# Kernel tuning notes

Measured on AMD Instinct MI355X. Metric: run time of the kernel, lower is better.

## Reference

```python
import jax, jax.numpy as jnp
import numpy as np

BN_EPS = 1e-5


def setup_inputs() -> dict:
    key = jax.random.key(0)
    k1, k2, k3, k4 = jax.random.split(key, 4)
    N, C, T, V, K = 64, 128, 300, 25, 3
    x = jax.random.normal(k1, (N, C, T, V), dtype=jnp.float32)
    A = jax.random.uniform(k2, (K, V, V), dtype=jnp.float32)
    # 1x1 conv weight (out_channels*K, in_channels) and bias
    W = jax.random.normal(k3, (C * K, C), dtype=jnp.float32) * 0.05
    b = jax.random.normal(k4, (C * K,), dtype=jnp.float32) * 0.05
    gamma = jnp.ones((C,), dtype=jnp.float32)
    beta = jnp.zeros((C,), dtype=jnp.float32)
    return {"x": x, "A": A, "W": W, "b": b, "gamma": gamma, "beta": beta}


def reference(x, A, W, b, gamma, beta):
    N, C, T, V = x.shape
    K = A.shape[0]
    # 1x1 conv: expand channels C -> K*C
    y = jnp.einsum('nctv,oc->notv', x, W) + b[None, :, None, None]
    y = y.reshape(N, K, C, T, V)
    # graph aggregation over K adjacency matrices
    y = jnp.einsum('nkctv,kvw->nctw', y, A)
    # residual + relu
    y = jax.nn.relu(y + x)
    # BatchNorm2d (training mode): stats over (N, T, V) per channel, biased var
    mean = jnp.mean(y, axis=(0, 2, 3), keepdims=True)
    var = jnp.mean(jnp.square(y - mean), axis=(0, 2, 3), keepdims=True)
    out = gamma[None, :, None, None] * (y - mean) * jax.lax.rsqrt(var + BN_EPS) + beta[None, :, None, None]
    return out, A
```

## Files before the change

kernel.cpp:

```cpp
#include <hip/hip_runtime.h>
#include <cstdint>
#include <cstddef>

#define C_    128
#define T_    300
#define V_    25
#define TT    2
#define KA    3
#define KDIM  384
#define B2P   136
#define ALP   40
#define XTP   40
#define NSLOT 64
#define NTOT  64

#define ALBF_O 0
#define XT_O   3840
#define B2_O   14080
#define SH_TOT 22784

typedef __attribute__((ext_vector_type(8))) short short8;
typedef __attribute__((ext_vector_type(4))) short short4v;
typedef __attribute__((ext_vector_type(4))) float float4v;
typedef __attribute__((ext_vector_type(2))) float float2v;

__device__ __forceinline__ short f2bf(float f) {
  union { float f; uint32_t u; } v; v.f = f;
  uint32_t r = (v.u + 0x7FFFu + ((v.u >> 16) & 1u)) >> 16;
  return (short)(uint16_t)r;
}
__device__ __forceinline__ float bf2f(short s) {
  union { uint32_t u; float f; } v; v.u = ((uint32_t)(uint16_t)s) << 16;
  return v.f;
}

__global__ __launch_bounds__(256) void k0_prep(const float* __restrict__ W,
    const float* __restrict__ A, const float* __restrict__ b,
    short* __restrict__ W2, float* __restrict__ bias2, float* __restrict__ stats)
{
  int e = blockIdx.x * 256 + threadIdx.x;
  if (e < C_*KDIM) {
    int c = e / KDIM, kd = e % KDIM;
    int k = kd >> 7, c2 = kd & 127;
    W2[e] = f2bf(W[(k*C_ + c)*C_ + c2]);
  } else if (e < C_*KDIM + C_*32) {
    int i = e - C_*KDIM;
    int c = i >> 5, w = i & 31;
    float val = 0.f;
    if (w < V_) {
      for (int k = 0; k < KA; ++k) {
        float cs = 0.f;
        for (int v = 0; v < V_; ++v) cs += A[(k*V_ + v)*V_ + w];
        val += b[k*C_ + c] * cs;
      }
    }
    bias2[i] = val;
  } else if (e < C_*KDIM + C_*32 + 2*NSLOT*C_) {
    stats[e - (C_*KDIM + C_*32)] = 0.f;
  }
}

__global__ __launch_bounds__(256, 3) void k1_main(const float* __restrict__ x,
    const float* __restrict__ A, const short* __restrict__ W2,
    const float* __restrict__ bias2, float* __restrict__ ssum,
    float* __restrict__ ssq, float* __restrict__ out)
{
  __shared__ __align__(16) short SH[SH_TOT];
  short* Albf_ = SH + ALBF_O;
  short* xt_   = SH + XT_O;
  short* B2_   = SH + B2_O;

  const int tid  = threadIdx.x;
  const int lane = tid & 63;
  const int wid  = tid >> 6;
  const int l15  = lane & 15;
  const int quad = lane >> 4;
  const int nb = blockIdx.x;
  const int n  = nb / (T_/TT);
  const int tb = nb % (T_/TT);
  const int t0 = tb * TT;

  for (int i = tid; i < KA*32*ALP; i += 256) {
    int k = i / (32*ALP);
    int rem = i % (32*ALP);
    int w = rem / ALP;
    int v = rem % ALP;
    float a = (w < V_ && v < V_) ? A[(k*V_ + v)*V_ + w] : 0.f;
    Albf_[i] = f2bf(a);
  }
  for (int i = tid; i < TT*C_*15; i += 256) {
    int t = i / (C_*15);
    int r = i % (C_*15);
    int c = r / 15;
    int v = V_ + (r % 15);
    xt_[t*5120 + c*XTP + v] = 0;
  }
  {
    const float* xb = x + (((size_t)n*C_)*T_ + t0)*V_;
    for (int p = tid; p < 3200; p += 256) {
      int c = (p*5243) >> 17;
      int r = p - c*25;
      float2v xv = *(const float2v*)(xb + (size_t)c*(T_*V_) + 2*r);
      int j0 = 2*r;
      { int j = j0;   int t = (j >= V_); int v = j - t*V_; xt_[t*5120 + c*XTP + v] = f2bf(xv[0]); }
      { int j = j0+1; int t = (j >= V_); int v = j - t*V_; xt_[t*5120 + c*XTP + v] = f2bf(xv[1]); }
    }
  }
  __syncthreads();

  const int mh = wid >> 1;
  const int tW = wid & 1;
  const int wm = wid >> 1;
  const int wn = wid & 1;

  float4v acc[4][2];
  #pragma unroll
  for (int mi = 0; mi < 4; ++mi)
    #pragma unroll
    for (int ni = 0; ni < 2; ++ni)
      acc[mi][ni] = (float4v){0.f, 0.f, 0.f, 0.f};

  short8 w2r[4][4];
  const short* w2base = W2 + (size_t)(wm*64 + l15)*KDIM + quad*8;

  for (int k = 0; k < KA; ++k) {
    #pragma unroll
    for (int ks = 0; ks < 4; ++ks)
      #pragma unroll
      for (int mi = 0; mi < 4; ++mi)
        w2r[ks][mi] = *(const short8*)(w2base + (size_t)mi*16*KDIM + k*C_ + ks*32);

    {
      short8 bf0 = *(const short8*)&Albf_[k*1280 + l15*ALP + quad*8];
      short8 bf1 = *(const short8*)&Albf_[k*1280 + (16 + l15)*ALP + quad*8];
      #pragma unroll
      for (int mi4 = 0; mi4 < 4; ++mi4) {
        int m8 = mh*4 + mi4;
        short8 af = *(const short8*)&xt_[tW*5120 + (m8*16 + l15)*XTP + quad*8];
        int c2 = m8*16 + quad*4;
        #pragma unroll
        for (int ni = 0; ni < 2; ++ni) {
          float4v s1 = {0.f, 0.f, 0.f, 0.f};
          s1 = __builtin_amdgcn_mfma_f32_16x16x32_bf16(af, ni ? bf1 : bf0, s1, 0, 0, 0);
          short4v sv;
          sv[0] = f2bf(s1[0]); sv[1] = f2bf(s1[1]);
          sv[2] = f2bf(s1[2]); sv[3] = f2bf(s1[3]);
          int pos = tW*32 + ni*16 + l15;
          *(short4v*)&B2_[pos*B2P + c2] = sv;
        }
      }
    }
    __syncthreads();

    #pragma unroll
    for (int ks = 0; ks < 4; ++ks) {
      short8 b0 = *(const short8*)&B2_[(wn*32 + l15)*B2P + ks*32 + quad*8];
      short8 b1 = *(const short8*)&B2_[(wn*32 + 16 + l15)*B2P + ks*32 + quad*8];
      #pragma unroll
      for (int mi = 0; mi < 4; ++mi) {
        acc[mi][0] = __builtin_amdgcn_mfma_f32_16x16x32_bf16(w2r[ks][mi], b0, acc[mi][0], 0, 0, 0);
        acc[mi][1] = __builtin_amdgcn_mfma_f32_16x16x32_bf16(w2r[ks][mi], b1, acc[mi][1], 0, 0, 0);
      }
    }
    if (k < KA-1) __syncthreads();
  }

  float lsum[4][4], lsq[4][4];
  #pragma unroll
  for (int a1 = 0; a1 < 4; ++a1)
    #pragma unroll
    for (int a2 = 0; a2 < 4; ++a2) { lsum[a1][a2] = 0.f; lsq[a1][a2] = 0.f; }

  #pragma unroll
  for (int ni = 0; ni < 2; ++ni) {
    int pos = wn*32 + ni*16 + l15;
    int t = pos >> 5;
    int w = pos & 31;
    if (w < V_) {
      #pragma unroll
      for (int mi = 0; mi < 4; ++mi) {
        int cb = wm*64 + mi*16 + quad*4;
        #pragma unroll
        for (int r = 0; r < 4; ++r) {
          int cc = cb + r;
          float z = acc[mi][ni][r] + bias2[cc*32 + w];
          z += bf2f(xt_[t*5120 + cc*XTP + w]);
          z = fmaxf(z, 0.f);
          acc[mi][ni][r] = z;
          lsum[mi][r] += z;
          lsq[mi][r]  += z*z;
        }
      }
    }
  }

  __syncthreads();
  float* Zs = (float*)SH;

  #pragma unroll
  for (int ni = 0; ni < 2; ++ni) {
    int pos = wn*32 + ni*16 + l15;
    int t = pos >> 5;
    int w = pos & 31;
    if (w < V_) {
      #pragma unroll
      for (int mi = 0; mi < 4; ++mi) {
        int cb = wm*64 + mi*16 + quad*4;
        #pragma unroll
        for (int r = 0; r < 4; ++r) {
          Zs[(cb + r)*50 + t*V_ + w] = acc[mi][ni][r];
        }
      }
    }
  }
  __syncthreads();

  {
    float* ob = out + (((size_t)n*C_)*T_ + t0)*V_;
    for (int p = tid; p < 3200; p += 256) {
      int c = (p*5243) >> 17;
      int r = p - c*25;
      float2v zz = *(const float2v*)&Zs[c*50 + 2*r];
      *(float2v*)(ob + (size_t)c*(T_*V_) + 2*r) = zz;
    }
  }

  int slot = nb & (NSLOT - 1);
  #pragma unroll
  for (int mi = 0; mi < 4; ++mi) {
    #pragma unroll
    for (int r = 0; r < 4; ++r) {
      float s = lsum[mi][r];
      float q = lsq[mi][r];
      #pragma unroll
      for (int m = 1; m <= 8; m <<= 1) {
        s += __shfl_xor(s, m, 64);
        q += __shfl_xor(q, m, 64);
      }
      if (l15 == 0) {
        int cc = wm*64 + mi*16 + quad*4 + r;
        atomicAdd(&ssum[slot*C_ + cc], s);
        atomicAdd(&ssq[slot*C_ + cc], q);
      }
    }
  }
}

__global__ __launch_bounds__(256) void k2_stats(const float* __restrict__ ssum,
    const float* __restrict__ ssq, const float* __restrict__ gamma,
    const float* __restrict__ beta, const float* __restrict__ A,
    float* __restrict__ sscale, float* __restrict__ sshift, float* __restrict__ outA)
{
  int id = blockIdx.x * 256 + threadIdx.x;
  if (id < C_) {
    float s = 0.f, q = 0.f;
    for (int sl = 0; sl < NSLOT; ++sl) { s += ssum[sl*C_ + id]; q += ssq[sl*C_ + id]; }
    const float cnt = 480000.f;
    float mean = s / cnt;
    float var  = q / cnt - mean*mean;
    float inv  = rsqrtf(var + 1e-5f);
    float sc   = gamma[id] * inv;
    sscale[id] = sc;
    sshift[id] = beta[id] - mean * sc;
  } else if (id < C_ + KA*V_*V_) {
    int i = id - C_;
    outA[i] = A[i];
  }
}

__global__ __launch_bounds__(256) void k3_bn(float* __restrict__ out,
    const float* __restrict__ sscale, const float* __restrict__ sshift)
{
  __shared__ float s_sc[C_], s_sh[C_];
  int tid = threadIdx.x;
  if (tid < C_) s_sc[tid] = sscale[tid];
  else          s_sh[tid - C_] = sshift[tid - C_];
  __syncthreads();

  int n = blockIdx.x / 75;
  int chunk = blockIdx.x % 75;
  float* base = out + (size_t)n*C_*T_*V_ + chunk*100;

  int f = tid;
  #pragma unroll 4
  for (int it = 0; it < 12; ++it, f += 256) {
    int c = (f*5243) >> 17;
    int r = f - c*25;
    float4v* p = (float4v*)(base + (size_t)c*(T_*V_) + 4*r);
    float4v v = *p;
    float sc = s_sc[c], sh = s_sh[c];
    v[0] = v[0]*sc + sh; v[1] = v[1]*sc + sh;
    v[2] = v[2]*sc + sh; v[3] = v[3]*sc + sh;
    *p = v;
  }
  if (f < 3200) {
    int c = (f*5243) >> 17;
    int r = f - c*25;
    float4v* p = (float4v*)(base + (size_t)c*(T_*V_) + 4*r);
    float4v v = *p;
    float sc = s_sc[c], sh = s_sh[c];
    v[0] = v[0]*sc + sh; v[1] = v[1]*sc + sh;
    v[2] = v[2]*sc + sh; v[3] = v[3]*sc + sh;
    *p = v;
  }
}

extern "C" void kernel_launch(void* const* d_in, const int* in_sizes, int n_in,
                              void* d_out, int out_size, void* d_ws, size_t ws_size,
                              hipStream_t stream)
{
  const float* x     = (const float*)d_in[0];
  const float* A     = (const float*)d_in[1];
  const float* W     = (const float*)d_in[2];
  const float* b     = (const float*)d_in[3];
  const float* gamma = (const float*)d_in[4];
  const float* beta  = (const float*)d_in[5];
  float* out = (float*)d_out;

  short* W2    = (short*)d_ws;
  float* bias2 = (float*)((char*)d_ws + 98304);
  float* stats = (float*)((char*)d_ws + 114688);
  float* ssum   = stats;
  float* ssq    = stats + NSLOT*C_;
  float* sscale = stats + 2*NSLOT*C_;
  float* sshift = sscale + C_;
  float* outA = out + (size_t)NTOT*C_*T_*V_;

  k0_prep <<<272,   256, 0, stream>>>(W, A, b, W2, bias2, stats);
  k1_main <<<9600,  256, 0, stream>>>(x, A, W2, bias2, ssum, ssq, out);
  k2_stats<<<8,     256, 0, stream>>>(ssum, ssq, gamma, beta, A, sscale, sshift, outA);
  k3_bn   <<<4800,  256, 0, stream>>>(out, sscale, sshift);
}
```

Baseline: 889.9 us.

## Keep graph-aggregation result in registers via lane shuffles, drop LDS staging buffer

```diff
diff --git a/kernel.cpp b/kernel.cpp
--- a/kernel.cpp
+++ b/kernel.cpp
@@ -8,7 +8,6 @@
 #define TT    2
 #define KA    3
 #define KDIM  384
-#define B2P   136
 #define ALP   40
 #define XTP   40
 #define NSLOT 64
@@ -16,11 +15,9 @@
 
 #define ALBF_O 0
 #define XT_O   3840
-#define B2_O   14080
-#define SH_TOT 22784
+#define SH_TOT 14080
 
 typedef __attribute__((ext_vector_type(8))) short short8;
-typedef __attribute__((ext_vector_type(4))) short short4v;
 typedef __attribute__((ext_vector_type(4))) float float4v;
 typedef __attribute__((ext_vector_type(2))) float float2v;
 
@@ -32,6 +29,9 @@
 __device__ __forceinline__ float bf2f(short s) {
   union { uint32_t u; float f; } v; v.u = ((uint32_t)(uint16_t)s) << 16;
   return v.f;
+}
+__device__ __forceinline__ uint32_t pk2(float lo, float hi) {
+  return (uint32_t)(uint16_t)f2bf(lo) | ((uint32_t)(uint16_t)f2bf(hi) << 16);
 }
 
 __global__ __launch_bounds__(256) void k0_prep(const float* __restrict__ W,
@@ -60,7 +60,7 @@
   }
 }
 
-__global__ __launch_bounds__(256, 3) void k1_main(const float* __restrict__ x,
+__global__ __launch_bounds__(256, 4) void k1_main(const float* __restrict__ x,
     const float* __restrict__ A, const short* __restrict__ W2,
     const float* __restrict__ bias2, float* __restrict__ ssum,
     float* __restrict__ ssq, float* __restrict__ out)
@@ -68,7 +68,6 @@
   __shared__ __align__(16) short SH[SH_TOT];
   short* Albf_ = SH + ALBF_O;
   short* xt_   = SH + XT_O;
-  short* B2_   = SH + B2_O;
 
   const int tid  = threadIdx.x;
   const int lane = tid & 63;
@@ -108,8 +107,6 @@
   }
   __syncthreads();
 
-  const int mh = wid >> 1;
-  const int tW = wid & 1;
   const int wm = wid >> 1;
   const int wn = wid & 1;
 
@@ -120,49 +117,49 @@
     for (int ni = 0; ni < 2; ++ni)
       acc[mi][ni] = (float4v){0.f, 0.f, 0.f, 0.f};
 
-  short8 w2r[4][4];
   const short* w2base = W2 + (size_t)(wm*64 + l15)*KDIM + quad*8;
-
-  for (int k = 0; k < KA; ++k) {
-    #pragma unroll
-    for (int ks = 0; ks < 4; ++ks)
+  const int s0 = ((quad & 1) << 5) + l15;
+  const int s1 = s0 + 16;
+  const int hi = quad >> 1;
+
+  #pragma unroll 2
+  for (int kc = 0; kc < 12; ++kc) {
+    const int k  = kc >> 2;
+    const int cb = (kc & 3) * 32;
+    const int kb = k*C_ + cb;
+
+    short8 w2f[4];
+    #pragma unroll
+    for (int mi = 0; mi < 4; ++mi)
+      w2f[mi] = *(const short8*)(w2base + (size_t)mi*16*KDIM + kb);
+
+    short8 afA = *(const short8*)&xt_[wn*5120 + (cb + l15)*XTP + quad*8];
+    short8 afB = *(const short8*)&xt_[wn*5120 + (cb + 16 + l15)*XTP + quad*8];
+
+    #pragma unroll
+    for (int ni = 0; ni < 2; ++ni) {
+      short8 bfk = *(const short8*)&Albf_[k*1280 + (ni*16 + l15)*ALP + quad*8];
+      float4v dA = {0.f,0.f,0.f,0.f}, dB = {0.f,0.f,0.f,0.f};
+      dA = __builtin_amdgcn_mfma_f32_16x16x32_bf16(afA, bfk, dA, 0, 0, 0);
+      dB = __builtin_amdgcn_mfma_f32_16x16x32_bf16(afB, bfk, dB, 0, 0, 0);
+
+      int pA0 = (int)pk2(dA[0], dA[1]), pA1 = (int)pk2(dA[2], dA[3]);
+      int pB0 = (int)pk2(dB[0], dB[1]), pB1 = (int)pk2(dB[2], dB[3]);
+
+      int a0 = __shfl(pA0, s0), a1 = __shfl(pA1, s0);
+      int a2 = __shfl(pA0, s1), a3 = __shfl(pA1, s1);
+      int b0 = __shfl(pB0, s0), b1 = __shfl(pB1, s0);
+      int b2 = __shfl(pB0, s1), b3 = __shfl(pB1, s1);
+      union { short8 s; int u[4]; } bf;
+      bf.u[0] = hi ? b0 : a0;
+      bf.u[1] = hi ? b1 : a1;
+      bf.u[2] = hi ? b2 : a2;
+      bf.u[3] = hi ? b3 : a3;
+
       #pragma unroll
       for (int mi = 0; mi < 4; ++mi)
-        w2r[ks][mi] = *(const short8*)(w2base + (size_t)mi*16*KDIM + k*C_ + ks*32);
-
-    {
-      short8 bf0 = *(const short8*)&Albf_[k*1280 + l15*ALP + quad*8];
-      short8 bf1 = *(const short8*)&Albf_[k*1280 + (16 + l15)*ALP + quad*8];
-      #pragma unroll
-      for (int mi4 = 0; mi4 < 4; ++mi4) {
-        int m8 = mh*4 + mi4;
-        short8 af = *(const short8*)&xt_[tW*5120 + (m8*16 + l15)*XTP + quad*8];
-        int c2 = m8*16 + quad*4;
-        #pragma unroll
-        for (int ni = 0; ni < 2; ++ni) {
-          float4v s1 = {0.f, 0.f, 0.f, 0.f};
-          s1 = __builtin_amdgcn_mfma_f32_16x16x32_bf16(af, ni ? bf1 : bf0, s1, 0, 0, 0);
-          short4v sv;
-          sv[0] = f2bf(s1[0]); sv[1] = f2bf(s1[1]);
-          sv[2] = f2bf(s1[2]); sv[3] = f2bf(s1[3]);
-          int pos = tW*32 + ni*16 + l15;
-          *(short4v*)&B2_[pos*B2P + c2] = sv;
-        }
-      }
-    }
-    __syncthreads();
-
-    #pragma unroll
-    for (int ks = 0; ks < 4; ++ks) {
-      short8 b0 = *(const short8*)&B2_[(wn*32 + l15)*B2P + ks*32 + quad*8];
-      short8 b1 = *(const short8*)&B2_[(wn*32 + 16 + l15)*B2P + ks*32 + quad*8];
-      #pragma unroll
-      for (int mi = 0; mi < 4; ++mi) {
-        acc[mi][0] = __builtin_amdgcn_mfma_f32_16x16x32_bf16(w2r[ks][mi], b0, acc[mi][0], 0, 0, 0);
-        acc[mi][1] = __builtin_amdgcn_mfma_f32_16x16x32_bf16(w2r[ks][mi], b1, acc[mi][1], 0, 0, 0);
-      }
-    }
-    if (k < KA-1) __syncthreads();
+        acc[mi][ni] = __builtin_amdgcn_mfma_f32_16x16x32_bf16(w2f[mi], bf.s, acc[mi][ni], 0, 0, 0);
+    }
   }
 
   float lsum[4][4], lsq[4][4];
@@ -171,57 +168,27 @@
     #pragma unroll
     for (int a2 = 0; a2 < 4; ++a2) { lsum[a1][a2] = 0.f; lsq[a1][a2] = 0.f; }
 
+  const int tG = t0 + wn;
+  float* obase = out + (size_t)n*(C_*T_*V_) + (size_t)tG*V_;
+
   #pragma unroll
   for (int ni = 0; ni < 2; ++ni) {
-    int pos = wn*32 + ni*16 + l15;
-    int t = pos >> 5;
-    int w = pos & 31;
-    if (w < V_) {
+    int w = ni*16 + l15;
+    bool act = (w < V_);
+    #pragma unroll
+    for (int mi = 0; mi < 4; ++mi) {
       #pragma unroll
-      for (int mi = 0; mi < 4; ++mi) {
-        int cb = wm*64 + mi*16 + quad*4;
-        #pragma unroll
-        for (int r = 0; r < 4; ++r) {
-          int cc = cb + r;
-          float z = acc[mi][ni][r] + bias2[cc*32 + w];
-          z += bf2f(xt_[t*5120 + cc*XTP + w]);
-          z = fmaxf(z, 0.f);
-          acc[mi][ni][r] = z;
+      for (int r = 0; r < 4; ++r) {
+        int cc = wm*64 + mi*16 + quad*4 + r;
+        float z = acc[mi][ni][r] + bias2[cc*32 + w];
+        z += bf2f(xt_[wn*5120 + cc*XTP + w]);
+        z = fmaxf(z, 0.f);
+        if (act) {
+          obase[(size_t)cc*(T_*V_) + w] = z;
           lsum[mi][r] += z;
           lsq[mi][r]  += z*z;
         }
       }
-    }
-  }
-
-  __syncthreads();
-  float* Zs = (float*)SH;
-
-  #pragma unroll
-  for (int ni = 0; ni < 2; ++ni) {
-    int pos = wn*32 + ni*16 + l15;
-    int t = pos >> 5;
-    int w = pos & 31;
-    if (w < V_) {
-      #pragma unroll
-      for (int mi = 0; mi < 4; ++mi) {
-        int cb = wm*64 + mi*16 + quad*4;
-        #pragma unroll
-        for (int r = 0; r < 4; ++r) {
-          Zs[(cb + r)*50 + t*V_ + w] = acc[mi][ni][r];
-        }
-      }
-    }
-  }
-  __syncthreads();
-
-  {
-    float* ob = out + (((size_t)n*C_)*T_ + t0)*V_;
-    for (int p = tid; p < 3200; p += 256) {
-      int c = (p*5243) >> 17;
-      int r = p - c*25;
-      float2v zz = *(const float2v*)&Zs[c*50 + 2*r];
-      *(float2v*)(ob + (size_t)c*(T_*V_) + 2*r) = zz;
     }
   }
 
```

Result: faster. 851.6 us (-4.3%).
